# Performance work log

Measured on AMD Instinct MI355X. Metric: run time of the kernel, lower is better.

## Reference

```python
import jax, jax.numpy as jnp
import numpy as np
import math

# ---- static configuration (mirrors init_kwargs) ----
NQ = 8            # n_qubits (main register)
NA = 2            # n_ancilla = ceil(log2(n_select))
NSEL = 4          # n_select
DEG = 3           # degree
LAYERS = 2        # n_ansatz_layers
KLOC = 2          # k_local
LATENT = 128
B = 256
NROTS = 4 * NQ * LAYERS          # 64
GROUPS = [(s, s + 1) for s in range(NQ - KLOC + 1)]  # sliding 2-local -> 7 groups
NOBS = len(GROUPS)
KDIM = 2 ** KLOC                  # 4
C64 = jnp.complex64
TWO_PI = 2.0 * math.pi

CNOT = jnp.array([[1, 0, 0, 0], [0, 1, 0, 0], [0, 0, 0, 1], [0, 0, 1, 0]], dtype=C64)

# ---- gate matrices (theta may be traced) ----
def ry_mat(th):
    c = jnp.cos(th / 2).astype(C64); s = jnp.sin(th / 2).astype(C64)
    return jnp.stack([jnp.stack([c, -s]), jnp.stack([s, c])])

def rz_mat(th):
    return jnp.diag(jnp.stack([jnp.exp(-0.5j * th), jnp.exp(0.5j * th)])).astype(C64)

def crx_mat(th):
    c = jnp.cos(th / 2).astype(C64); isn = (-1j * jnp.sin(th / 2)).astype(C64)
    one = jnp.ones((), C64)
    m = jnp.zeros((4, 4), C64)
    m = m.at[0, 0].set(one).at[1, 1].set(one)
    m = m.at[2, 2].set(c).at[3, 3].set(c).at[2, 3].set(isn).at[3, 2].set(isn)
    return m

# ---- state-vector gate application (state: (2,)*rank, wire = axis) ----
def apply_1q(state, U, w):
    return jnp.moveaxis(jnp.tensordot(U, state, axes=((1,), (w,))), 0, w)

def apply_2q(state, U, w0, w1):
    st = jnp.tensordot(U.reshape(2, 2, 2, 2), state, axes=((2, 3), (w0, w1)))
    return jnp.moveaxis(st, (0, 1), (w0, w1))

def _sim14_ops(nq, layers):
    ops, idx = [], 0
    for _ in range(layers):
        for i in range(nq):
            ops.append(("ry", (i,), idx)); idx += 1
        for i in range(nq - 1, -1, -1):
            ops.append(("crx", (i, (i + 1) % nq), idx)); idx += 1
        for i in range(nq):
            ops.append(("ry", (i,), idx)); idx += 1
        for i in [nq - 1] + list(range(nq - 1)):
            ops.append(("crx", (i, (i - 1) % nq), idx)); idx += 1
    return ops

def apply_sim14(state, p, layers, adjoint=False):
    ops = _sim14_ops(NQ, layers)
    seq = list(reversed(ops)) if adjoint else ops
    sgn = -1.0 if adjoint else 1.0
    for kind, ws, idx in seq:
        th = sgn * p[idx]
        if kind == "ry":
            state = apply_1q(state, ry_mat(th), ws[0])
        else:
            state = apply_2q(state, crx_mat(th), ws[0], ws[1])
    return state

def pcphase(state, phi):
    # e^{+i phi} on ancilla=|0..0> subspace (first 2^NQ states in (anc, main) ordering), e^{-i phi} elsewhere
    sr = state.reshape(2 ** NQ, 2 ** NA)
    ph = jnp.where(jnp.arange(2 ** NA) == 0, jnp.exp(1j * phi), jnp.exp(-1j * phi)).astype(C64)
    return (sr * ph[None, :]).reshape(state.shape)

def prepare(state, prep_p, adjoint=False):
    if not adjoint:
        for ly in range(NA):          # n_prep_layers == n_ancilla
            for qi in range(NA):
                state = apply_1q(state, ry_mat(prep_p[ly, qi, 0]), NQ + qi)
                state = apply_1q(state, rz_mat(prep_p[ly, qi, 1]), NQ + qi)
            for i in range(NA - 1):
                state = apply_2q(state, CNOT, NQ + i, NQ + i + 1)
    else:
        for ly in reversed(range(NA)):
            for i in reversed(range(NA - 1)):
                state = apply_2q(state, CNOT, NQ + i, NQ + i + 1)
            for qi in reversed(range(NA)):
                state = apply_1q(state, rz_mat(-prep_p[ly, qi, 1]), NQ + qi)
                state = apply_1q(state, ry_mat(-prep_p[ly, qi, 0]), NQ + qi)
    return state

def select(state, ts, adjoint=False):
    # ancilla wires (NQ, NQ+1) are the trailing axes; flattened index == control value s
    sr = state.reshape((2,) * NQ + (2 ** NA,))
    for s in range(NSEL):
        sub = apply_sim14(sr[..., s], ts[s], LAYERS, adjoint=adjoint)
        sr = sr.at[..., s].set(sub)
    return sr.reshape(state.shape)

def create_hermitian(A, Bp, D, N):
    h = jnp.zeros((N, N), C64)
    count = 0
    for i in range(1, N):
        h = h.at[i - 1, i - 1].set(D[i].astype(C64))
        for j in range(i):
            h = h.at[i, j].set((A[count + j] + 1j * Bp[count + j]).astype(C64))
        count += i
    return h + h.conj().T

def simulate(ts, prep_p, sig, qff, H_all):
    # ts: (NSEL, NROTS) for one batch element
    state = jnp.zeros((2,) * (NQ + NA), C64).at[(0,) * (NQ + NA)].set(1.0)
    state = pcphase(state, sig[0])
    for k in range(DEG):
        state = prepare(state, prep_p)
        state = select(state, ts, adjoint=(k % 2 == 1))
        state = prepare(state, prep_p, adjoint=True)
        state = pcphase(state, sig[k + 1])
    state = apply_sim14(state, qff, 1)
    es = []
    for w, (a, b) in enumerate(GROUPS):
        hpsi = apply_2q(state, H_all[w], a, b)
        es.append(jnp.real(jnp.vdot(state, hpsi)))
    return jnp.stack(es).astype(jnp.float32)  # (NOBS,)

def linear(x, w, b):
    return x @ w.T + b

def sinusoidal_embedding(t, dim):
    half = dim // 2
    freqs = jnp.exp(-math.log(10000.0) * jnp.arange(half, dtype=jnp.float32) / half)
    args = t[:, None] * freqs[None]
    return jnp.concatenate([jnp.cos(args), jnp.sin(args)], axis=-1)

def _forward(z_t, t, te_w1, te_b1, te_w2, te_b2, ip_w1, ip_b1, ip_w2, ip_b2,
             prep_params, signal_angles, qff_params, A_obs, B_obs, D_obs, head_w, head_b):
    t_emb = sinusoidal_embedding(t, LATENT)
    t_emb = linear(jax.nn.silu(linear(t_emb, te_w1, te_b1)), te_w2, te_b2)
    h = jnp.concatenate([z_t, t_emb], axis=-1)
    h = linear(jax.nn.silu(linear(h, ip_w1, ip_b1)), ip_w2, ip_b2)
    ts = jax.nn.sigmoid(h).reshape(z_t.shape[0], NSEL, NROTS) * TWO_PI
    H_all = jax.vmap(lambda a, b, d: create_hermitian(a, b, d, KDIM))(A_obs, B_obs, D_obs)  # (NOBS,4,4)
    expvals = jax.vmap(simulate, in_axes=(0, None, None, None, None))(
        ts, prep_params, signal_angles, qff_params, H_all)  # (B, NOBS)
    return linear(expvals, head_w, head_b)  # (B, LATENT)

def setup_inputs() -> dict:
    key = jax.random.key(0)
    ks = jax.random.split(key, 16)
    def n(k, shape, s=0.05):
        return s * jax.random.normal(k, shape, jnp.float32)
    return {
        "z_t": jax.random.normal(ks[0], (B, LATENT), jnp.float32),
        "t": jax.random.uniform(ks[1], (B,), jnp.float32),
        "te_w1": n(ks[2], (LATENT, LATENT)), "te_b1": jnp.zeros((LATENT,), jnp.float32),
        "te_w2": n(ks[3], (LATENT, LATENT)), "te_b2": jnp.zeros((LATENT,), jnp.float32),
        "ip_w1": n(ks[4], (2 * LATENT, 2 * LATENT)), "ip_b1": jnp.zeros((2 * LATENT,), jnp.float32),
        "ip_w2": n(ks[5], (NSEL * NROTS, 2 * LATENT)), "ip_b2": jnp.zeros((NSEL * NROTS,), jnp.float32),
        "prep_params": 0.1 * jax.random.normal(ks[6], (NA, NA, 2), jnp.float32),
        "signal_angles": 0.1 * jax.random.normal(ks[7], (DEG + 1,), jnp.float32),
        "qff_params": jax.random.uniform(ks[8], (4 * NQ,), jnp.float32),
        "A_obs": 2.0 * jax.random.normal(ks[9], (NOBS, KDIM * (KDIM - 1) // 2), jnp.float32),
        "B_obs": 2.0 * jax.random.normal(ks[10], (NOBS, KDIM * (KDIM - 1) // 2), jnp.float32),
        "D_obs": 2.0 * jax.random.normal(ks[11], (NOBS, KDIM), jnp.float32),
        "head_w": n(ks[12], (LATENT, NOBS)), "head_b": jnp.zeros((LATENT,), jnp.float32),
    }

def reference(z_t, t, te_w1, te_b1, te_w2, te_b2, ip_w1, ip_b1, ip_w2, ip_b2,
              prep_params, signal_angles, qff_params, A_obs, B_obs, D_obs, head_w, head_b):
    return _forward(z_t, t, te_w1, te_b1, te_w2, te_b2, ip_w1, ip_b1, ip_w2, ip_b2,
                    prep_params, signal_angles, qff_params, A_obs, B_obs, D_obs, head_w, head_b)
```

## Files before the change

### kernel.cpp

```cpp
#include <hip/hip_runtime.h>
#include <math.h>

#define NOBS 7
#define TWO_PI_F 6.283185307179586f


constexpr int REG_MASK(int w)  { return w==6 ? 2 : w==7 ? 1 : 0; }
constexpr int LANE_MASK(int w) { return w<=5 ? (1 << (5-w)) : 0; }

__device__ __forceinline__ float2 cmul(float2 a, float2 b) {
  return make_float2(a.x*b.x - a.y*b.y, a.x*b.y + a.y*b.x);
}
__device__ __forceinline__ float2 cmulc(float2 a, float2 b) {
  return make_float2(a.x*b.x + a.y*b.y, a.y*b.x - a.x*b.y);
}
__device__ __forceinline__ float2 cadd(float2 a, float2 b) {
  return make_float2(a.x + b.x, a.y + b.y);
}


template<int W>
__device__ __forceinline__ void ry_gate(float* vr, float* vi, int lane,
                                        const float2* tab, int idx, float sg)
{
  float2 cs = tab[idx];
  float c = cs.x, s = sg * cs.y;
  if constexpr (REG_MASK(W) != 0) {
    constexpr int m = REG_MASK(W);
#pragma unroll
    for (int r = 0; r < 4; ++r) {
      if (r & m) continue;
      const int r1 = r | m;
      float a0 = vr[r], a1 = vr[r1];
      vr[r]  = c*a0 - s*a1;  vr[r1] = s*a0 + c*a1;
      float b0 = vi[r], b1 = vi[r1];
      vi[r]  = c*b0 - s*b1;  vi[r1] = s*b0 + c*b1;
    }
  } else {
    constexpr int LM = LANE_MASK(W);
    const float ls = (lane & LM) ? s : -s;
#pragma unroll
    for (int r = 0; r < 4; ++r) {
      float pr = __shfl_xor(vr[r], LM, 64);
      float pi = __shfl_xor(vi[r], LM, 64);
      vr[r] = c*vr[r] + ls*pr;
      vi[r] = c*vi[r] + ls*pi;
    }
  }
}

template<int WC, int WT>
__device__ __forceinline__ void crx_gate(float* vr, float* vi, int lane,
                                         const float2* tab, int idx, float sg)
{
  float2 cs = tab[idx];
  float c = cs.x, s = sg * cs.y;
  constexpr int MC = REG_MASK(WC), LC = LANE_MASK(WC);
  constexpr int MT = REG_MASK(WT), LT = LANE_MASK(WT);
  if constexpr (MC != 0 && MT != 0) {
#pragma unroll
    for (int r = 0; r < 4; ++r) {
      if (!(r & MC) || (r & MT)) continue;
      const int r1 = r | MT;
      float xr = vr[r], xi = vi[r], yr = vr[r1], yi = vi[r1];
      vr[r]  = c*xr + s*yi;  vi[r]  = c*xi - s*yr;
      vr[r1] = c*yr + s*xi;  vi[r1] = c*yi - s*xr;
    }
  } else if constexpr (MC != 0) {
#pragma unroll
    for (int r = 0; r < 4; ++r) {
      if (!(r & MC)) continue;
      float pr = __shfl_xor(vr[r], LT, 64);
      float pi = __shfl_xor(vi[r], LT, 64);
      vr[r] = c*vr[r] + s*pi;
      vi[r] = c*vi[r] - s*pr;
    }
  } else if constexpr (MT != 0) {
    const bool act = (lane & LC) != 0;
#pragma unroll
    for (int r = 0; r < 4; ++r) {
      if (r & MT) continue;
      const int r1 = r | MT;
      float xr = vr[r], xi = vi[r], yr = vr[r1], yi = vi[r1];
      float nxr = c*xr + s*yi, nxi = c*xi - s*yr;
      float nyr = c*yr + s*xi, nyi = c*yi - s*xr;
      vr[r]  = act ? nxr : xr;  vi[r]  = act ? nxi : xi;
      vr[r1] = act ? nyr : yr;  vi[r1] = act ? nyi : yi;
    }
  } else {
    const bool act = (lane & LC) != 0;
#pragma unroll
    for (int r = 0; r < 4; ++r) {
      float pr = __shfl_xor(vr[r], LT, 64);
      float pi = __shfl_xor(vi[r], LT, 64);
      float nr = c*vr[r] + s*pi;
      float ni = c*vi[r] - s*pr;
      vr[r] = act ? nr : vr[r];
      vi[r] = act ? ni : vi[r];
    }
  }
}


__device__ __forceinline__ void sim14_fwd(float* vr, float* vi, int lane,
                                          const float2* tab, int off, float sg)
{
  ry_gate<0>(vr,vi,lane,tab,off+0,sg);  ry_gate<1>(vr,vi,lane,tab,off+1,sg);
  ry_gate<2>(vr,vi,lane,tab,off+2,sg);  ry_gate<3>(vr,vi,lane,tab,off+3,sg);
  ry_gate<4>(vr,vi,lane,tab,off+4,sg);  ry_gate<5>(vr,vi,lane,tab,off+5,sg);
  ry_gate<6>(vr,vi,lane,tab,off+6,sg);  ry_gate<7>(vr,vi,lane,tab,off+7,sg);
  crx_gate<7,0>(vr,vi,lane,tab,off+8,sg);  crx_gate<6,7>(vr,vi,lane,tab,off+9,sg);
  crx_gate<5,6>(vr,vi,lane,tab,off+10,sg); crx_gate<4,5>(vr,vi,lane,tab,off+11,sg);
  crx_gate<3,4>(vr,vi,lane,tab,off+12,sg); crx_gate<2,3>(vr,vi,lane,tab,off+13,sg);
  crx_gate<1,2>(vr,vi,lane,tab,off+14,sg); crx_gate<0,1>(vr,vi,lane,tab,off+15,sg);
  ry_gate<0>(vr,vi,lane,tab,off+16,sg); ry_gate<1>(vr,vi,lane,tab,off+17,sg);
  ry_gate<2>(vr,vi,lane,tab,off+18,sg); ry_gate<3>(vr,vi,lane,tab,off+19,sg);
  ry_gate<4>(vr,vi,lane,tab,off+20,sg); ry_gate<5>(vr,vi,lane,tab,off+21,sg);
  ry_gate<6>(vr,vi,lane,tab,off+22,sg); ry_gate<7>(vr,vi,lane,tab,off+23,sg);
  crx_gate<7,6>(vr,vi,lane,tab,off+24,sg); crx_gate<0,7>(vr,vi,lane,tab,off+25,sg);
  crx_gate<1,0>(vr,vi,lane,tab,off+26,sg); crx_gate<2,1>(vr,vi,lane,tab,off+27,sg);
  crx_gate<3,2>(vr,vi,lane,tab,off+28,sg); crx_gate<4,3>(vr,vi,lane,tab,off+29,sg);
  crx_gate<5,4>(vr,vi,lane,tab,off+30,sg); crx_gate<6,5>(vr,vi,lane,tab,off+31,sg);
}

__device__ __forceinline__ void sim14_adj(float* vr, float* vi, int lane,
                                          const float2* tab, int off)
{
  const float sg = -1.f;
  crx_gate<6,5>(vr,vi,lane,tab,off+31,sg); crx_gate<5,4>(vr,vi,lane,tab,off+30,sg);
  crx_gate<4,3>(vr,vi,lane,tab,off+29,sg); crx_gate<3,2>(vr,vi,lane,tab,off+28,sg);
  crx_gate<2,1>(vr,vi,lane,tab,off+27,sg); crx_gate<1,0>(vr,vi,lane,tab,off+26,sg);
  crx_gate<0,7>(vr,vi,lane,tab,off+25,sg); crx_gate<7,6>(vr,vi,lane,tab,off+24,sg);
  ry_gate<7>(vr,vi,lane,tab,off+23,sg); ry_gate<6>(vr,vi,lane,tab,off+22,sg);
  ry_gate<5>(vr,vi,lane,tab,off+21,sg); ry_gate<4>(vr,vi,lane,tab,off+20,sg);
  ry_gate<3>(vr,vi,lane,tab,off+19,sg); ry_gate<2>(vr,vi,lane,tab,off+18,sg);
  ry_gate<1>(vr,vi,lane,tab,off+17,sg); ry_gate<0>(vr,vi,lane,tab,off+16,sg);
  crx_gate<0,1>(vr,vi,lane,tab,off+15,sg); crx_gate<1,2>(vr,vi,lane,tab,off+14,sg);
  crx_gate<2,3>(vr,vi,lane,tab,off+13,sg); crx_gate<3,4>(vr,vi,lane,tab,off+12,sg);
  crx_gate<4,5>(vr,vi,lane,tab,off+11,sg); crx_gate<5,6>(vr,vi,lane,tab,off+10,sg);
  crx_gate<6,7>(vr,vi,lane,tab,off+9,sg);  crx_gate<7,0>(vr,vi,lane,tab,off+8,sg);
  ry_gate<7>(vr,vi,lane,tab,off+7,sg); ry_gate<6>(vr,vi,lane,tab,off+6,sg);
  ry_gate<5>(vr,vi,lane,tab,off+5,sg); ry_gate<4>(vr,vi,lane,tab,off+4,sg);
  ry_gate<3>(vr,vi,lane,tab,off+3,sg); ry_gate<2>(vr,vi,lane,tab,off+2,sg);
  ry_gate<1>(vr,vi,lane,tab,off+1,sg); ry_gate<0>(vr,vi,lane,tab,off+0,sg);
}


__global__ __launch_bounds__(256) void qsvt_kernel(
    const float* __restrict__ z_t, const float* __restrict__ t,
    const float* __restrict__ te_w1, const float* __restrict__ te_b1,
    const float* __restrict__ te_w2, const float* __restrict__ te_b2,
    const float* __restrict__ ip_w1, const float* __restrict__ ip_b1,
    const float* __restrict__ ip_w2, const float* __restrict__ ip_b2,
    const float* __restrict__ prep_p, const float* __restrict__ sig,
    const float* __restrict__ qff, const float* __restrict__ A_obs,
    const float* __restrict__ B_obs, const float* __restrict__ D_obs,
    const float* __restrict__ head_w, const float* __restrict__ head_b,
    float* __restrict__ out)
{
  __shared__ __align__(16) float emb[128];
  __shared__ __align__(16) float y1[128];
  __shared__ __align__(16) float hbuf[256];
  __shared__ __align__(16) float h1[256];
  __shared__ __align__(16) float2 seltab[256];
  __shared__ __align__(16) float2 qtab[32];
  __shared__ __align__(16) float2 xbuf[64*17];
  __shared__ __align__(16) float dumpR[4][256];
  __shared__ __align__(16) float dumpI[4][256];
  __shared__ float redbuf[NOBS][4];

  const int tid  = threadIdx.x;
  const int lane = tid & 63;
  const int s    = tid >> 6;
  const int b    = blockIdx.x;

  if (tid < 64) {
    float tb = t[b];
    float fr = expf(-logf(10000.f) * (float)tid / 64.f);
    float arg = tb * fr;
    emb[tid]      = cosf(arg);
    emb[64 + tid] = sinf(arg);
  }
  __syncthreads();
  if (tid < 128) {
    const float4* w4 = (const float4*)(te_w1 + tid * 128);
    const float4* e4 = (const float4*)emb;
    float acc = te_b1[tid];
#pragma unroll 8
    for (int j = 0; j < 32; ++j) {
      float4 w = w4[j], e = e4[j];
      acc += w.x*e.x + w.y*e.y + w.z*e.z + w.w*e.w;
    }
    y1[tid] = acc / (1.f + expf(-acc));
  }
  __syncthreads();
  if (tid < 128) {
    const float4* w4 = (const float4*)(te_w2 + tid * 128);
    const float4* e4 = (const float4*)y1;
    float acc = te_b2[tid];
#pragma unroll 8
    for (int j = 0; j < 32; ++j) {
      float4 w = w4[j], e = e4[j];
      acc += w.x*e.x + w.y*e.y + w.z*e.z + w.w*e.w;
    }
    hbuf[128 + tid] = acc;
  } else {
    hbuf[tid - 128] = z_t[b * 128 + (tid - 128)];
  }
  __syncthreads();
  {
    const float4* w4 = (const float4*)(ip_w1 + tid * 256);
    const float4* e4 = (const float4*)hbuf;
    float acc = ip_b1[tid];
#pragma unroll 8
    for (int j = 0; j < 64; ++j) {
      float4 w = w4[j], e = e4[j];
      acc += w.x*e.x + w.y*e.y + w.z*e.z + w.w*e.w;
    }
    h1[tid] = acc / (1.f + expf(-acc));
  }
  __syncthreads();
  {
    const float4* w4 = (const float4*)(ip_w2 + tid * 256);
    const float4* e4 = (const float4*)h1;
    float acc = ip_b2[tid];
#pragma unroll 8
    for (int j = 0; j < 64; ++j) {
      float4 w = w4[j], e = e4[j];
      acc += w.x*e.x + w.y*e.y + w.z*e.z + w.w*e.w;
    }
    float theta = (1.f / (1.f + expf(-acc))) * TWO_PI_F;
    seltab[tid] = make_float2(cosf(0.5f * theta), sinf(0.5f * theta));
  }
  if (tid < 32) {
    float a = qff[tid];
    qtab[tid] = make_float2(cosf(0.5f * a), sinf(0.5f * a));
  }

  float2 Ga[2][2][2], Gb[2][2][2];
#pragma unroll
  for (int ly = 0; ly < 2; ++ly) {
#pragma unroll
    for (int qi = 0; qi < 2; ++qi) {
      float y = prep_p[ly*4 + qi*2 + 0], z = prep_p[ly*4 + qi*2 + 1];
      float cy = cosf(0.5f*y), sy = sinf(0.5f*y), cz = cosf(0.5f*z), sz = sinf(0.5f*z);
      float2 g00 = make_float2( cy*cz, -cy*sz);
      float2 g01 = make_float2(-sy*cz,  sy*sz);
      float2 g10 = make_float2( sy*cz,  sy*sz);
      float2 g11 = make_float2( cy*cz,  cy*sz);
      if (qi == 0) { Ga[ly][0][0]=g00; Ga[ly][0][1]=g01; Ga[ly][1][0]=g10; Ga[ly][1][1]=g11; }
      else         { Gb[ly][0][0]=g00; Gb[ly][0][1]=g01; Gb[ly][1][0]=g10; Gb[ly][1][1]=g11; }
    }
  }
  float2 M[2][4][4];
#pragma unroll
  for (int ly = 0; ly < 2; ++ly) {
    float2 T[4][4];
#pragma unroll
    for (int i = 0; i < 4; ++i)
#pragma unroll
      for (int j = 0; j < 4; ++j)
        T[i][j] = cmul(Ga[ly][i>>1][j>>1], Gb[ly][i&1][j&1]);
#pragma unroll
    for (int j = 0; j < 4; ++j) {
      M[ly][0][j] = T[0][j]; M[ly][1][j] = T[1][j];
      M[ly][2][j] = T[3][j]; M[ly][3][j] = T[2][j];
    }
  }
  float2 U[4][4];
#pragma unroll
  for (int i = 0; i < 4; ++i)
#pragma unroll
    for (int j = 0; j < 4; ++j) {
      float2 acc = make_float2(0.f, 0.f);
#pragma unroll
      for (int kk = 0; kk < 4; ++kk) acc = cadd(acc, cmul(M[1][i][kk], M[0][kk][j]));
      U[i][j] = acc;
    }
  float2 Urow[4], Ucol[4];
#pragma unroll
  for (int j = 0; j < 4; ++j) {
    Urow[j] = s==0 ? U[0][j] : s==1 ? U[1][j] : s==2 ? U[2][j] : U[3][j];
    Ucol[j] = s==0 ? U[j][0] : s==1 ? U[j][1] : s==2 ? U[j][2] : U[j][3];
  }
  float sg0 = sig[0], sg1 = sig[1], sg2 = sig[2], sg3 = sig[3];
  float c1 = cosf(sg1), s1v = sinf(sg1);
  float c2 = cosf(sg2), s2v = sinf(sg2);
  float c3 = cosf(sg3), s3v = sinf(sg3);
  float2 R1[4], R2[4], RF[4];
  {
    float s3s = (s == 0) ? s3v : -s3v;
    float2 d3 = make_float2(c3, s3s);
#pragma unroll
    for (int sp = 0; sp < 4; ++sp) {
      float2 a1 = make_float2(0.f, 0.f), a2 = make_float2(0.f, 0.f);
#pragma unroll
      for (int j = 0; j < 4; ++j) {
        float2 uspj = sp==0 ? U[0][j] : sp==1 ? U[1][j] : sp==2 ? U[2][j] : U[3][j];
        float2 tt = cmulc(Urow[j], uspj);
        float sj = (j == 0) ? 1.f : -1.f;
        a1 = cadd(a1, cmul(tt, make_float2(c1, sj*s1v)));
        a2 = cadd(a2, cmul(tt, make_float2(c2, sj*s2v)));
      }
      R1[sp] = a1; R2[sp] = a2;
      RF[sp] = cmul(d3, make_float2(Ucol[sp].x, -Ucol[sp].y));
    }
  }
  __syncthreads();

  float vr[4], vi[4];
  {
    float2 a0 = cmul(Urow[0], make_float2(cosf(sg0), sinf(sg0)));
#pragma unroll
    for (int r = 0; r < 4; ++r) { vr[r] = 0.f; vi[r] = 0.f; }
    if (lane == 0) { vr[0] = a0.x; vi[0] = a0.y; }
  }
  const float2* stab = &seltab[s * 64];

  sim14_fwd(vr, vi, lane, stab, 0, 1.f);
  sim14_fwd(vr, vi, lane, stab, 32, 1.f);
  {
#pragma unroll
    for (int r = 0; r < 4; ++r) xbuf[lane*17 + r*4 + s] = make_float2(vr[r], vi[r]);
    __syncthreads();
#pragma unroll
    for (int r = 0; r < 4; ++r) {
      const float2* p = &xbuf[lane*17 + r*4];
      float2 o = cmul(R1[0], p[0]);
      o = cadd(o, cmul(R1[1], p[1]));
      o = cadd(o, cmul(R1[2], p[2]));
      o = cadd(o, cmul(R1[3], p[3]));
      vr[r] = o.x; vi[r] = o.y;
    }
    __syncthreads();
  }
  sim14_adj(vr, vi, lane, stab, 32);
  sim14_adj(vr, vi, lane, stab, 0);
  {
#pragma unroll
    for (int r = 0; r < 4; ++r) xbuf[lane*17 + r*4 + s] = make_float2(vr[r], vi[r]);
    __syncthreads();
#pragma unroll
    for (int r = 0; r < 4; ++r) {
      const float2* p = &xbuf[lane*17 + r*4];
      float2 o = cmul(R2[0], p[0]);
      o = cadd(o, cmul(R2[1], p[1]));
      o = cadd(o, cmul(R2[2], p[2]));
      o = cadd(o, cmul(R2[3], p[3]));
      vr[r] = o.x; vi[r] = o.y;
    }
    __syncthreads();
  }
  sim14_fwd(vr, vi, lane, stab, 0, 1.f);
  sim14_fwd(vr, vi, lane, stab, 32, 1.f);
  {
#pragma unroll
    for (int r = 0; r < 4; ++r) xbuf[lane*17 + r*4 + s] = make_float2(vr[r], vi[r]);
    __syncthreads();
#pragma unroll
    for (int r = 0; r < 4; ++r) {
      const float2* p = &xbuf[lane*17 + r*4];
      float2 o = cmul(RF[0], p[0]);
      o = cadd(o, cmul(RF[1], p[1]));
      o = cadd(o, cmul(RF[2], p[2]));
      o = cadd(o, cmul(RF[3], p[3]));
      vr[r] = o.x; vi[r] = o.y;
    }
    __syncthreads();
  }
  sim14_fwd(vr, vi, lane, qtab, 0, 1.f);

  *(float4*)&dumpR[s][lane*4] = make_float4(vr[0], vr[1], vr[2], vr[3]);
  *(float4*)&dumpI[s][lane*4] = make_float4(vi[0], vi[1], vi[2], vi[3]);

#pragma unroll
  for (int w = 0; w < NOBS; ++w) {
    const int pb = 6 - w;
    int g = lane;
    int ib = ((g >> pb) << (pb + 2)) | (g & ((1 << pb) - 1));
    float xr[4], xi[4];
#pragma unroll
    for (int i = 0; i < 4; ++i) { xr[i] = dumpR[s][ib + (i << pb)]; xi[i] = dumpI[s][ib + (i << pb)]; }
    float hd0 = 2.f * D_obs[w*4 + 1];
    float hd1 = 2.f * D_obs[w*4 + 2];
    float hd2 = 2.f * D_obs[w*4 + 3];
    float a = hd0 * (xr[0]*xr[0] + xi[0]*xi[0])
            + hd1 * (xr[1]*xr[1] + xi[1]*xi[1])
            + hd2 * (xr[2]*xr[2] + xi[2]*xi[2]);
    const int oi[6] = {1, 2, 2, 3, 3, 3};
    const int oj[6] = {0, 0, 1, 0, 1, 2};
#pragma unroll
    for (int k2 = 0; k2 < 6; ++k2) {
      int i = oi[k2], j = oj[k2];
      float rr = xr[i]*xr[j] + xi[i]*xi[j];
      float ii = xr[i]*xi[j] - xi[i]*xr[j];
      a += 2.f * (A_obs[w*6 + k2]*rr - B_obs[w*6 + k2]*ii);
    }
#pragma unroll
    for (int o = 32; o > 0; o >>= 1) a += __shfl_xor(a, o, 64);
    if (lane == 0) redbuf[w][s] = a;
  }
  __syncthreads();

  if (tid < 128) {
    float acc = head_b[tid];
#pragma unroll
    for (int w = 0; w < NOBS; ++w) {
      float ev = redbuf[w][0] + redbuf[w][1] + redbuf[w][2] + redbuf[w][3];
      acc += ev * head_w[tid*NOBS + w];
    }
    out[b * 128 + tid] = acc;
  }
}

extern "C" void kernel_launch(void* const* d_in, const int* in_sizes, int n_in,
                              void* d_out, int out_size, void* d_ws, size_t ws_size,
                              hipStream_t stream) {
  (void)n_in; (void)out_size; (void)d_ws; (void)ws_size;
  const float* z_t    = (const float*)d_in[0];
  const float* t      = (const float*)d_in[1];
  const float* te_w1  = (const float*)d_in[2];
  const float* te_b1  = (const float*)d_in[3];
  const float* te_w2  = (const float*)d_in[4];
  const float* te_b2  = (const float*)d_in[5];
  const float* ip_w1  = (const float*)d_in[6];
  const float* ip_b1  = (const float*)d_in[7];
  const float* ip_w2  = (const float*)d_in[8];
  const float* ip_b2  = (const float*)d_in[9];
  const float* prep_p = (const float*)d_in[10];
  const float* sig    = (const float*)d_in[11];
  const float* qff    = (const float*)d_in[12];
  const float* A_obs  = (const float*)d_in[13];
  const float* B_obs  = (const float*)d_in[14];
  const float* D_obs  = (const float*)d_in[15];
  const float* head_w = (const float*)d_in[16];
  const float* head_b = (const float*)d_in[17];
  float* out = (float*)d_out;

  int B = in_sizes[1];
  qsvt_kernel<<<B, 256, 0, stream>>>(
      z_t, t, te_w1, te_b1, te_w2, te_b2, ip_w1, ip_b1, ip_w2, ip_b2,
      prep_p, sig, qff, A_obs, B_obs, D_obs, head_w, head_b, out);
}
```

Measured before the change: 144.3 us.

## Coalesce MLP matvecs, use DPP lane swaps, fast sincos, stage constants in LDS

The four MLP matvecs are restructured so that 8 lanes cooperate on each output row with coalesced float4 loads and a shuffle/DPP reduction. The aim is to replace strided per-thread row reads that waste memory bandwidth. Xor-1 and xor-2 lane exchanges in the gates and reductions now use DPP quad permutes instead of ds_bpermute shuffles. Accurate sin/cos/exp calls become fast intrinsics, and observable and head weights are preloaded into shared memory. Using the fast intrinsics risks a small loss of numerical accuracy.

```diff
diff --git a/kernel.cpp b/kernel.cpp
--- a/kernel.cpp
+++ b/kernel.cpp
@@ -3,10 +3,21 @@
 
 #define NOBS 7
 #define TWO_PI_F 6.283185307179586f
+#define PI_F 3.14159265358979f
 
 
 constexpr int REG_MASK(int w)  { return w==6 ? 2 : w==7 ? 1 : 0; }
 constexpr int LANE_MASK(int w) { return w<=5 ? (1 << (5-w)) : 0; }
+
+template<int LM>
+__device__ __forceinline__ float lane_xor(float x) {
+  if constexpr (LM == 1)
+    return __int_as_float(__builtin_amdgcn_mov_dpp(__float_as_int(x), 0xB1, 0xF, 0xF, true));
+  else if constexpr (LM == 2)
+    return __int_as_float(__builtin_amdgcn_mov_dpp(__float_as_int(x), 0x4E, 0xF, 0xF, true));
+  else
+    return __shfl_xor(x, LM, 64);
+}
 
 __device__ __forceinline__ float2 cmul(float2 a, float2 b) {
   return make_float2(a.x*b.x - a.y*b.y, a.x*b.y + a.y*b.x);
@@ -41,8 +52,8 @@
     const float ls = (lane & LM) ? s : -s;
 #pragma unroll
     for (int r = 0; r < 4; ++r) {
-      float pr = __shfl_xor(vr[r], LM, 64);
-      float pi = __shfl_xor(vi[r], LM, 64);
+      float pr = lane_xor<LM>(vr[r]);
+      float pi = lane_xor<LM>(vi[r]);
       vr[r] = c*vr[r] + ls*pr;
       vi[r] = c*vi[r] + ls*pi;
     }
@@ -70,8 +81,8 @@
 #pragma unroll
     for (int r = 0; r < 4; ++r) {
       if (!(r & MC)) continue;
-      float pr = __shfl_xor(vr[r], LT, 64);
-      float pi = __shfl_xor(vi[r], LT, 64);
+      float pr = lane_xor<LT>(vr[r]);
+      float pi = lane_xor<LT>(vi[r]);
       vr[r] = c*vr[r] + s*pi;
       vi[r] = c*vi[r] - s*pr;
     }
@@ -91,8 +102,8 @@
     const bool act = (lane & LC) != 0;
 #pragma unroll
     for (int r = 0; r < 4; ++r) {
-      float pr = __shfl_xor(vr[r], LT, 64);
-      float pi = __shfl_xor(vi[r], LT, 64);
+      float pr = lane_xor<LT>(vr[r]);
+      float pi = lane_xor<LT>(vi[r]);
       float nr = c*vr[r] + s*pi;
       float ni = c*vi[r] - s*pr;
       vr[r] = act ? nr : vr[r];
@@ -146,6 +157,44 @@
 }
 
 
+template<int IN, int NP, int MODE>
+__device__ __forceinline__ void mlp_layer(const float* __restrict__ W,
+    const float* __restrict__ bias, const float* xl, float* yl,
+    int rbase, int lane)
+{
+  const int sub = lane & 7;
+  const int g   = lane >> 3;
+#pragma unroll
+  for (int p = 0; p < NP; ++p) {
+    const int row = rbase + p * 8 + g;
+    const float4* w4 = (const float4*)(W + row * IN) + sub;
+    const float4* x4 = (const float4*)xl + sub;
+    float acc = 0.f;
+#pragma unroll
+    for (int it = 0; it < IN / 32; ++it) {
+      float4 w = w4[it * 8], e = x4[it * 8];
+      acc += w.x*e.x + w.y*e.y + w.z*e.z + w.w*e.w;
+    }
+    acc += lane_xor<1>(acc);
+    acc += lane_xor<2>(acc);
+    acc += __shfl_xor(acc, 4, 64);
+    if (sub == 0) {
+      float a = acc + bias[row];
+      if constexpr (MODE == 0) {
+        yl[row] = a / (1.f + __expf(-a));
+      } else if constexpr (MODE == 1) {
+        yl[row] = a;
+      } else {
+        float th = PI_F / (1.f + __expf(-a));
+        float sn, cn;
+        __sincosf(th, &sn, &cn);
+        ((float2*)yl)[row] = make_float2(cn, sn);
+      }
+    }
+  }
+}
+
+
 __global__ __launch_bounds__(256) void qsvt_kernel(
     const float* __restrict__ z_t, const float* __restrict__ t,
     const float* __restrict__ te_w1, const float* __restrict__ te_b1,
@@ -168,74 +217,47 @@
   __shared__ __align__(16) float dumpR[4][256];
   __shared__ __align__(16) float dumpI[4][256];
   __shared__ float redbuf[NOBS][4];
+  __shared__ float hdc[NOBS][3], hxc[NOBS][6], hyc[NOBS][6];
+  __shared__ __align__(16) float shw[128*NOBS];
+  __shared__ __align__(16) float shb[128];
 
   const int tid  = threadIdx.x;
   const int lane = tid & 63;
   const int s    = tid >> 6;
   const int b    = blockIdx.x;
 
-  if (tid < 64) {
-    float tb = t[b];
-    float fr = expf(-logf(10000.f) * (float)tid / 64.f);
-    float arg = tb * fr;
-    emb[tid]      = cosf(arg);
-    emb[64 + tid] = sinf(arg);
-  }
-  __syncthreads();
   if (tid < 128) {
-    const float4* w4 = (const float4*)(te_w1 + tid * 128);
-    const float4* e4 = (const float4*)emb;
-    float acc = te_b1[tid];
-#pragma unroll 8
-    for (int j = 0; j < 32; ++j) {
-      float4 w = w4[j], e = e4[j];
-      acc += w.x*e.x + w.y*e.y + w.z*e.z + w.w*e.w;
-    }
-    y1[tid] = acc / (1.f + expf(-acc));
-  }
-  __syncthreads();
-  if (tid < 128) {
-    const float4* w4 = (const float4*)(te_w2 + tid * 128);
-    const float4* e4 = (const float4*)y1;
-    float acc = te_b2[tid];
-#pragma unroll 8
-    for (int j = 0; j < 32; ++j) {
-      float4 w = w4[j], e = e4[j];
-      acc += w.x*e.x + w.y*e.y + w.z*e.z + w.w*e.w;
-    }
-    hbuf[128 + tid] = acc;
-  } else {
-    hbuf[tid - 128] = z_t[b * 128 + (tid - 128)];
-  }
-  __syncthreads();
-  {
-    const float4* w4 = (const float4*)(ip_w1 + tid * 256);
-    const float4* e4 = (const float4*)hbuf;
-    float acc = ip_b1[tid];
-#pragma unroll 8
-    for (int j = 0; j < 64; ++j) {
-      float4 w = w4[j], e = e4[j];
-      acc += w.x*e.x + w.y*e.y + w.z*e.z + w.w*e.w;
-    }
-    h1[tid] = acc / (1.f + expf(-acc));
-  }
-  __syncthreads();
-  {
-    const float4* w4 = (const float4*)(ip_w2 + tid * 256);
-    const float4* e4 = (const float4*)h1;
-    float acc = ip_b2[tid];
-#pragma unroll 8
-    for (int j = 0; j < 64; ++j) {
-      float4 w = w4[j], e = e4[j];
-      acc += w.x*e.x + w.y*e.y + w.z*e.z + w.w*e.w;
-    }
-    float theta = (1.f / (1.f + expf(-acc))) * TWO_PI_F;
-    seltab[tid] = make_float2(cosf(0.5f * theta), sinf(0.5f * theta));
-  }
-  if (tid < 32) {
-    float a = qff[tid];
-    qtab[tid] = make_float2(cosf(0.5f * a), sinf(0.5f * a));
-  }
+    int j = tid & 63;
+    float fr = __expf(-9.210340371976184f * (float)j / 64.f);
+    float arg = t[b] * fr;
+    float sn, cn;
+    __sincosf(arg, &sn, &cn);
+    emb[tid] = (tid < 64) ? cn : sn;
+  } else if (tid < 160) {
+    int j = tid - 128;
+    float sn, cn;
+    __sincosf(0.5f * qff[j], &sn, &cn);
+    qtab[j] = make_float2(cn, sn);
+  }
+  __syncthreads();
+
+  mlp_layer<128, 4, 0>(te_w1, te_b1, emb, y1, s * 32, lane);
+  if (tid < 128) hbuf[tid] = z_t[b * 128 + tid];
+  __syncthreads();
+
+  mlp_layer<128, 4, 1>(te_w2, te_b2, y1, hbuf + 128, s * 32, lane);
+  __syncthreads();
+
+  mlp_layer<256, 8, 0>(ip_w1, ip_b1, hbuf, h1, s * 64, lane);
+  __syncthreads();
+
+  mlp_layer<256, 8, 2>(ip_w2, ip_b2, h1, (float*)seltab, s * 64, lane);
+
+  if (tid < NOBS * 6)      { hxc[tid/6][tid%6] = A_obs[tid]; hyc[tid/6][tid%6] = B_obs[tid]; }
+  else if (tid >= 64 && tid < 64 + NOBS*3) { int q = tid - 64; hdc[q/3][q%3] = 2.f * D_obs[(q/3)*4 + (q%3) + 1]; }
+#pragma unroll
+  for (int i = tid; i < 128*NOBS; i += 256) shw[i] = head_w[i];
+  if (tid < 128) shb[tid] = head_b[tid];
 
   float2 Ga[2][2][2], Gb[2][2][2];
 #pragma unroll
@@ -243,7 +265,9 @@
 #pragma unroll
     for (int qi = 0; qi < 2; ++qi) {
       float y = prep_p[ly*4 + qi*2 + 0], z = prep_p[ly*4 + qi*2 + 1];
-      float cy = cosf(0.5f*y), sy = sinf(0.5f*y), cz = cosf(0.5f*z), sz = sinf(0.5f*z);
+      float cy, sy, cz, sz;
+      __sincosf(0.5f*y, &sy, &cy);
+      __sincosf(0.5f*z, &sz, &cz);
       float2 g00 = make_float2( cy*cz, -cy*sz);
       float2 g01 = make_float2(-sy*cz,  sy*sz);
       float2 g10 = make_float2( sy*cz,  sy*sz);
@@ -284,9 +308,10 @@
     Ucol[j] = s==0 ? U[j][0] : s==1 ? U[j][1] : s==2 ? U[j][2] : U[j][3];
   }
   float sg0 = sig[0], sg1 = sig[1], sg2 = sig[2], sg3 = sig[3];
-  float c1 = cosf(sg1), s1v = sinf(sg1);
-  float c2 = cosf(sg2), s2v = sinf(sg2);
-  float c3 = cosf(sg3), s3v = sinf(sg3);
+  float c1, s1v, c2, s2v, c3, s3v;
+  __sincosf(sg1, &s1v, &c1);
+  __sincosf(sg2, &s2v, &c2);
+  __sincosf(sg3, &s3v, &c3);
   float2 R1[4], R2[4], RF[4];
   {
     float s3s = (s == 0) ? s3v : -s3v;
@@ -310,7 +335,9 @@
 
   float vr[4], vi[4];
   {
-    float2 a0 = cmul(Urow[0], make_float2(cosf(sg0), sinf(sg0)));
+    float s0n, c0n;
+    __sincosf(sg0, &s0n, &c0n);
+    float2 a0 = cmul(Urow[0], make_float2(c0n, s0n));
 #pragma unroll
     for (int r = 0; r < 4; ++r) { vr[r] = 0.f; vi[r] = 0.f; }
     if (lane == 0) { vr[0] = a0.x; vi[0] = a0.y; }
@@ -381,12 +408,9 @@
     float xr[4], xi[4];
 #pragma unroll
     for (int i = 0; i < 4; ++i) { xr[i] = dumpR[s][ib + (i << pb)]; xi[i] = dumpI[s][ib + (i << pb)]; }
-    float hd0 = 2.f * D_obs[w*4 + 1];
-    float hd1 = 2.f * D_obs[w*4 + 2];
-    float hd2 = 2.f * D_obs[w*4 + 3];
-    float a = hd0 * (xr[0]*xr[0] + xi[0]*xi[0])
-            + hd1 * (xr[1]*xr[1] + xi[1]*xi[1])
-            + hd2 * (xr[2]*xr[2] + xi[2]*xi[2]);
+    float a = hdc[w][0] * (xr[0]*xr[0] + xi[0]*xi[0])
+            + hdc[w][1] * (xr[1]*xr[1] + xi[1]*xi[1])
+            + hdc[w][2] * (xr[2]*xr[2] + xi[2]*xi[2]);
     const int oi[6] = {1, 2, 2, 3, 3, 3};
     const int oj[6] = {0, 0, 1, 0, 1, 2};
 #pragma unroll
@@ -394,20 +418,24 @@
       int i = oi[k2], j = oj[k2];
       float rr = xr[i]*xr[j] + xi[i]*xi[j];
       float ii = xr[i]*xi[j] - xi[i]*xr[j];
-      a += 2.f * (A_obs[w*6 + k2]*rr - B_obs[w*6 + k2]*ii);
-    }
-#pragma unroll
-    for (int o = 32; o > 0; o >>= 1) a += __shfl_xor(a, o, 64);
+      a += 2.f * (hxc[w][k2]*rr - hyc[w][k2]*ii);
+    }
+    a += __shfl_xor(a, 32, 64);
+    a += __shfl_xor(a, 16, 64);
+    a += __shfl_xor(a, 8, 64);
+    a += __shfl_xor(a, 4, 64);
+    a += lane_xor<2>(a);
+    a += lane_xor<1>(a);
     if (lane == 0) redbuf[w][s] = a;
   }
   __syncthreads();
 
   if (tid < 128) {
-    float acc = head_b[tid];
+    float acc = shb[tid];
 #pragma unroll
     for (int w = 0; w < NOBS; ++w) {
       float ev = redbuf[w][0] + redbuf[w][1] + redbuf[w][2] + redbuf[w][3];
-      acc += ev * head_w[tid*NOBS + w];
+      acc += ev * shw[tid*NOBS + w];
     }
     out[b * 128 + tid] = acc;
   }
```

New measurement: 128.8 us. 1.12x faster.
